# Kernel optimization log

Measured on AMD Instinct MI355X. Metric: run time of the kernel, lower is better.

Reference implementation:

```python
import jax, jax.numpy as jnp
import numpy as np

H, W, D = 160, 160, 16
VOXEL_SIZE = 0.4
VOL_MIN = np.array([-32.0, -32.0, -1.0], dtype=np.float32)
SCALE_MULTIPLIER = 3.0
N_GAUSS = 8192
CHUNK = 64


def setup_inputs() -> dict:
    key = jax.random.key(0)
    k1, k2, k3, k4, k5 = jax.random.split(key, 5)
    vol_min = jnp.asarray(VOL_MIN)
    vol_ext = jnp.array([64.0, 64.0, 6.4], dtype=jnp.float32)
    means3d = jax.random.uniform(k1, (N_GAUSS, 3), jnp.float32) * vol_ext + vol_min
    opacities = jax.random.uniform(k2, (N_GAUSS, 1), jnp.float32)
    # per-axis std devs: 0.2..0.8 m so 3-sigma footprint spans a handful of voxels
    scales = 0.2 + 0.6 * jax.random.uniform(k3, (N_GAUSS, 3), jnp.float32)
    rotations = jax.random.normal(k4, (N_GAUSS, 4), jnp.float32)
    features = jax.random.normal(k5, (N_GAUSS, 32), jnp.float32)
    return {"means3d": means3d, "opacities": opacities, "scales": scales,
            "rotations": rotations, "features": features}


def quat_to_rotmat(q):
    # q: [N,4] wxyz, normalized
    w, x, y, z = q[:, 0], q[:, 1], q[:, 2], q[:, 3]
    R = jnp.stack([
        jnp.stack([1 - 2 * (y * y + z * z), 2 * (x * y - w * z), 2 * (x * z + w * y)], -1),
        jnp.stack([2 * (x * y + w * z), 1 - 2 * (x * x + z * z), 2 * (y * z - w * x)], -1),
        jnp.stack([2 * (x * z - w * y), 2 * (y * z + w * x), 1 - 2 * (x * x + y * y)], -1),
    ], axis=-2)  # [N,3,3]
    return R


def _grid_coords():
    ii, jj, kk = jnp.meshgrid(jnp.arange(H), jnp.arange(W), jnp.arange(D), indexing="ij")
    idx = jnp.stack([ii, jj, kk], axis=-1).astype(jnp.float32)
    return (idx + 0.5) * VOXEL_SIZE + jnp.asarray(VOL_MIN)  # [H,W,D,3] voxel centers


def reference(means3d, opacities, scales, rotations, features):
    x = _grid_coords().reshape(-1, 3)  # [V,3]
    q = rotations / jnp.linalg.norm(rotations, axis=-1, keepdims=True)
    R = quat_to_rotmat(q)
    # covariance = R diag(s^2) R^T
    cov = jnp.einsum("nij,nj,nkj->nik", R, scales * scales, R)
    cov_inv = jnp.linalg.inv(cov)
    sigma = jnp.sqrt(jnp.diagonal(cov, axis1=1, axis2=2))  # [N,3]
    opac = opacities[:, 0]  # [N]
    n = means3d.shape[0]
    nchunks = n // CHUNK

    def chunked(a):
        return a.reshape(nchunks, CHUNK, *a.shape[1:])

    def step(acc, c):
        mu, op, sg, ci, ft = c
        diff = x[:, None, :] - mu[None, :, :]  # [V,CHUNK,3]
        maha = jnp.einsum("vci,cij,vcj->vc", diff, ci, diff)
        # local aggregation cutoff: within scale_multiplier * sigma box around mean
        mask = jnp.all(jnp.abs(diff) <= SCALE_MULTIPLIER * sg[None, :, :], axis=-1)
        w = op[None, :] * jnp.exp(-0.5 * maha) * mask  # [V,CHUNK]
        return acc + w @ ft, None

    acc0 = jnp.zeros((x.shape[0], features.shape[-1]), jnp.float32)
    xs = (chunked(means3d), chunked(opac), chunked(sigma), chunked(cov_inv), chunked(features))
    acc, _ = jax.lax.scan(step, acc0, xs)
    return acc.reshape(H, W, D, features.shape[-1])
```

## Files before the change

kernel.cpp:

```cpp
#include <hip/hip_runtime.h>

#define HH 160
#define WW 160
#define DD 16
#define NG 8192
#define VOXEL 0.4f

#define TTX 20
#define TTY 20
#define TTZ 4
#define NTILES (TTX * TTY * TTZ)
#define CAP 256


__global__ __launch_bounds__(64) void gv_precompute_bin(
    const float* __restrict__ means, const float* __restrict__ opac,
    const float* __restrict__ scales, const float* __restrict__ rots,
    float4* __restrict__ pack, int* __restrict__ tileCnt,
    int* __restrict__ tileList) {
  int g = blockIdx.x * 64 + threadIdx.x;
  if (g >= NG) return;
  float qw = rots[g * 4 + 0], qx = rots[g * 4 + 1];
  float qy = rots[g * 4 + 2], qz = rots[g * 4 + 3];
  float inv = rsqrtf(qw * qw + qx * qx + qy * qy + qz * qz);
  qw *= inv; qx *= inv; qy *= inv; qz *= inv;
  float R[3][3];
  R[0][0] = 1.f - 2.f * (qy * qy + qz * qz);
  R[0][1] = 2.f * (qx * qy - qw * qz);
  R[0][2] = 2.f * (qx * qz + qw * qy);
  R[1][0] = 2.f * (qx * qy + qw * qz);
  R[1][1] = 1.f - 2.f * (qx * qx + qz * qz);
  R[1][2] = 2.f * (qy * qz - qw * qx);
  R[2][0] = 2.f * (qx * qz - qw * qy);
  R[2][1] = 2.f * (qy * qz + qw * qx);
  R[2][2] = 1.f - 2.f * (qx * qx + qy * qy);
  float sx = scales[g * 3 + 0], sy = scales[g * 3 + 1], sz = scales[g * 3 + 2];
  float s2[3] = {sx * sx, sy * sy, sz * sz};
  float is2[3] = {1.f / s2[0], 1.f / s2[1], 1.f / s2[2]};
  float cov00 = 0.f, cov11 = 0.f, cov22 = 0.f;
  float ci00 = 0.f, ci01 = 0.f, ci02 = 0.f, ci11 = 0.f, ci12 = 0.f, ci22 = 0.f;
#pragma unroll
  for (int c = 0; c < 3; c++) {
    cov00 += R[0][c] * R[0][c] * s2[c];
    cov11 += R[1][c] * R[1][c] * s2[c];
    cov22 += R[2][c] * R[2][c] * s2[c];
    ci00 += R[0][c] * R[0][c] * is2[c];
    ci01 += R[0][c] * R[1][c] * is2[c];
    ci02 += R[0][c] * R[2][c] * is2[c];
    ci11 += R[1][c] * R[1][c] * is2[c];
    ci12 += R[1][c] * R[2][c] * is2[c];
    ci22 += R[2][c] * R[2][c] * is2[c];
  }
  float mx = means[g * 3 + 0], my = means[g * 3 + 1], mz = means[g * 3 + 2];
  float bx = 3.f * sqrtf(cov00), by = 3.f * sqrtf(cov11), bz = 3.f * sqrtf(cov22);
  float4* p = pack + (size_t)g * 4;
  p[0] = make_float4(mx, my, mz, opac[g]);
  p[1] = make_float4(bx, by, bz, ci00);
  p[2] = make_float4(ci01, ci02, ci11, ci12);
  p[3] = make_float4(ci22, 0.f, 0.f, 0.f);

  const float eps = 1e-4f;
  int i0 = (int)ceilf((mx - bx + 32.f) * 2.5f - 0.5f - eps);
  int i1 = (int)floorf((mx + bx + 32.f) * 2.5f - 0.5f + eps);
  int j0 = (int)ceilf((my - by + 32.f) * 2.5f - 0.5f - eps);
  int j1 = (int)floorf((my + by + 32.f) * 2.5f - 0.5f + eps);
  int k0 = (int)ceilf((mz - bz + 1.f) * 2.5f - 0.5f - eps);
  int k1 = (int)floorf((mz + bz + 1.f) * 2.5f - 0.5f + eps);
  i0 = max(i0, 0); i1 = min(i1, HH - 1);
  j0 = max(j0, 0); j1 = min(j1, WW - 1);
  k0 = max(k0, 0); k1 = min(k1, DD - 1);
  if (i0 > i1 || j0 > j1 || k0 > k1) return;
  int ti0 = i0 >> 3, ti1 = i1 >> 3;
  int tj0 = j0 >> 3, tj1 = j1 >> 3;
  int tk0 = k0 >> 2, tk1 = k1 >> 2;
  for (int ti = ti0; ti <= ti1; ti++)
    for (int tj = tj0; tj <= tj1; tj++)
      for (int tk = tk0; tk <= tk1; tk++) {
        int t = (ti * TTY + tj) * TTZ + tk;
        int pos = atomicAdd(&tileCnt[t], 1);
        if (pos < CAP) tileList[t * CAP + pos] = g;
      }
}

__global__ __launch_bounds__(256) void gv_voxelize(
    const float4* __restrict__ pack, const float4* __restrict__ feats,
    const int* __restrict__ tileCnt, const int* __restrict__ tileList,
    float4* __restrict__ out) {
  int tid = threadIdx.x;
  int dk = tid & 3, dj = (tid >> 2) & 7, di = tid >> 5;
  int tk = blockIdx.x, tj = blockIdx.y, ti = blockIdx.z;
  int i = ti * 8 + di, j = tj * 8 + dj, k = tk * 4 + dk;

  float px = (i + 0.5f) * VOXEL - 32.f;
  float py = (j + 0.5f) * VOXEL - 32.f;
  float pz = (k + 0.5f) * VOXEL - 1.f;

  int t = (ti * TTY + tj) * TTZ + tk;
  int cnt = tileCnt[t];
  cnt = min(cnt, CAP);
  const int* __restrict__ lst = tileList + t * CAP;

  float4 acc[8];
#pragma unroll
  for (int f = 0; f < 8; f++) acc[f] = make_float4(0.f, 0.f, 0.f, 0.f);

  int n = 0;
  for (; n + 2 <= cnt; n += 2) {
    int g0 = __builtin_amdgcn_readfirstlane(lst[n]);
    int g1 = __builtin_amdgcn_readfirstlane(lst[n + 1]);
    const float4* __restrict__ p0 = pack + (size_t)g0 * 4;
    const float4* __restrict__ p1 = pack + (size_t)g1 * 4;
    float4 a0 = p0[0], b0 = p0[1], c0 = p0[2], d0 = p0[3];
    float4 a1 = p1[0], b1 = p1[1], c1 = p1[2], d1 = p1[3];

    float dx0 = px - a0.x, dy0 = py - a0.y, dz0 = pz - a0.z;
    float dx1 = px - a1.x, dy1 = py - a1.y, dz1 = pz - a1.z;
    bool in0 = (fabsf(dx0) <= b0.x) & (fabsf(dy0) <= b0.y) & (fabsf(dz0) <= b0.z);
    bool in1 = (fabsf(dx1) <= b1.x) & (fabsf(dy1) <= b1.y) & (fabsf(dz1) <= b1.z);

    if (__any(in0)) {
      float maha = b0.w * dx0 * dx0 + c0.z * dy0 * dy0 + d0.x * dz0 * dz0 +
                   2.f * (c0.x * dx0 * dy0 + c0.y * dx0 * dz0 + c0.w * dy0 * dz0);
      float w = in0 ? a0.w * __expf(-0.5f * maha) : 0.f;
      const float4* __restrict__ fp = feats + (size_t)g0 * 8;
#pragma unroll
      for (int f = 0; f < 8; f++) {
        float4 fv = fp[f];
        acc[f].x += w * fv.x;
        acc[f].y += w * fv.y;
        acc[f].z += w * fv.z;
        acc[f].w += w * fv.w;
      }
    }
    if (__any(in1)) {
      float maha = b1.w * dx1 * dx1 + c1.z * dy1 * dy1 + d1.x * dz1 * dz1 +
                   2.f * (c1.x * dx1 * dy1 + c1.y * dx1 * dz1 + c1.w * dy1 * dz1);
      float w = in1 ? a1.w * __expf(-0.5f * maha) : 0.f;
      const float4* __restrict__ fp = feats + (size_t)g1 * 8;
#pragma unroll
      for (int f = 0; f < 8; f++) {
        float4 fv = fp[f];
        acc[f].x += w * fv.x;
        acc[f].y += w * fv.y;
        acc[f].z += w * fv.z;
        acc[f].w += w * fv.w;
      }
    }
  }
  if (n < cnt) {
    int gg = __builtin_amdgcn_readfirstlane(lst[n]);
    const float4* __restrict__ p = pack + (size_t)gg * 4;
    float4 pa = p[0], pb = p[1];
    float dx = px - pa.x, dy = py - pa.y, dz = pz - pa.z;
    bool in = (fabsf(dx) <= pb.x) & (fabsf(dy) <= pb.y) & (fabsf(dz) <= pb.z);
    if (__any(in)) {
      float4 pc = p[2], pd = p[3];
      float maha = pb.w * dx * dx + pc.z * dy * dy + pd.x * dz * dz +
                   2.f * (pc.x * dx * dy + pc.y * dx * dz + pc.w * dy * dz);
      float w = in ? pa.w * __expf(-0.5f * maha) : 0.f;
      const float4* __restrict__ fp = feats + (size_t)gg * 8;
#pragma unroll
      for (int f = 0; f < 8; f++) {
        float4 fv = fp[f];
        acc[f].x += w * fv.x;
        acc[f].y += w * fv.y;
        acc[f].z += w * fv.z;
        acc[f].w += w * fv.w;
      }
    }
  }

  size_t v = ((size_t)i * WW + j) * DD + k;
  float4* o = out + v * 8;
#pragma unroll
  for (int f = 0; f < 8; f++) o[f] = acc[f];
}

extern "C" void kernel_launch(void* const* d_in, const int* in_sizes, int n_in,
                              void* d_out, int out_size, void* d_ws, size_t ws_size,
                              hipStream_t stream) {
  const float* means  = (const float*)d_in[0];
  const float* opac   = (const float*)d_in[1];
  const float* scales = (const float*)d_in[2];
  const float* rots   = (const float*)d_in[3];
  const float4* feats = (const float4*)d_in[4];

  char* ws = (char*)d_ws;
  float4* pack   = (float4*)ws;
  int* tileCnt   = (int*)(ws + 512 * 1024);
  int* tileList  = (int*)(ws + 520 * 1024);

  hipMemsetAsync(tileCnt, 0, NTILES * sizeof(int), stream);
  gv_precompute_bin<<<128, 64, 0, stream>>>(means, opac, scales, rots,
                                            pack, tileCnt, tileList);
  dim3 grid(TTZ, TTY, TTX);
  gv_voxelize<<<grid, 256, 0, stream>>>(pack, feats, tileCnt, tileList,
                                        (float4*)d_out);
}
```

Measured before the change: 128.9 us.

## Bin gaussians into finer 4x4x4 tiles so each wavefront scans its own list

Gaussians are now binned into 4x4x4 voxel tiles instead of 8x8x4, and each 64-lane wavefront of the voxelize block maps to one of these finer tiles and reads its own per-tile list. Each wave therefore tests fewer gaussians that cannot reach its voxels, which cuts the per-candidate load and the culling check. In exchange the binning pass does more atomics and list writes, since each gaussian lands in more tiles. The per-tile capacity drops to 128, which could drop gaussians in dense tiles.

```diff
diff --git a/kernel.cpp b/kernel.cpp
--- a/kernel.cpp
+++ b/kernel.cpp
@@ -6,11 +6,15 @@
 #define NG 8192
 #define VOXEL 0.4f
 
+#define FTX 40
+#define FTY 40
+#define FTZ 4
+#define NFT (FTX * FTY * FTZ)
+#define CAP 128
+
 #define TTX 20
 #define TTY 20
 #define TTZ 4
-#define NTILES (TTX * TTY * TTZ)
-#define CAP 256
 
 
 __global__ __launch_bounds__(64) void gv_precompute_bin(
@@ -70,13 +74,13 @@
   j0 = max(j0, 0); j1 = min(j1, WW - 1);
   k0 = max(k0, 0); k1 = min(k1, DD - 1);
   if (i0 > i1 || j0 > j1 || k0 > k1) return;
-  int ti0 = i0 >> 3, ti1 = i1 >> 3;
-  int tj0 = j0 >> 3, tj1 = j1 >> 3;
+  int ti0 = i0 >> 2, ti1 = i1 >> 2;
+  int tj0 = j0 >> 2, tj1 = j1 >> 2;
   int tk0 = k0 >> 2, tk1 = k1 >> 2;
   for (int ti = ti0; ti <= ti1; ti++)
     for (int tj = tj0; tj <= tj1; tj++)
       for (int tk = tk0; tk <= tk1; tk++) {
-        int t = (ti * TTY + tj) * TTZ + tk;
+        int t = (ti * FTY + tj) * FTZ + tk;
         int pos = atomicAdd(&tileCnt[t], 1);
         if (pos < CAP) tileList[t * CAP + pos] = g;
       }
@@ -87,7 +91,10 @@
     const int* __restrict__ tileCnt, const int* __restrict__ tileList,
     float4* __restrict__ out) {
   int tid = threadIdx.x;
-  int dk = tid & 3, dj = (tid >> 2) & 7, di = tid >> 5;
+  int w = tid >> 6;
+  int wi = w >> 1, wj = w & 1;
+  int l = tid & 63;
+  int dk = l & 3, dj = wj * 4 + ((l >> 2) & 3), di = wi * 4 + (l >> 4);
   int tk = blockIdx.x, tj = blockIdx.y, ti = blockIdx.z;
   int i = ti * 8 + di, j = tj * 8 + dj, k = tk * 4 + dk;
 
@@ -95,8 +102,9 @@
   float py = (j + 0.5f) * VOXEL - 32.f;
   float pz = (k + 0.5f) * VOXEL - 1.f;
 
-  int t = (ti * TTY + tj) * TTZ + tk;
-  int cnt = tileCnt[t];
+  int sti = ti * 2 + wi, stj = tj * 2 + wj, stk = tk;
+  int t = __builtin_amdgcn_readfirstlane((sti * FTY + stj) * FTZ + stk);
+  int cnt = __builtin_amdgcn_readfirstlane(tileCnt[t]);
   cnt = min(cnt, CAP);
   const int* __restrict__ lst = tileList + t * CAP;
 
@@ -121,29 +129,29 @@
     if (__any(in0)) {
       float maha = b0.w * dx0 * dx0 + c0.z * dy0 * dy0 + d0.x * dz0 * dz0 +
                    2.f * (c0.x * dx0 * dy0 + c0.y * dx0 * dz0 + c0.w * dy0 * dz0);
-      float w = in0 ? a0.w * __expf(-0.5f * maha) : 0.f;
+      float wgt = in0 ? a0.w * __expf(-0.5f * maha) : 0.f;
       const float4* __restrict__ fp = feats + (size_t)g0 * 8;
 #pragma unroll
       for (int f = 0; f < 8; f++) {
         float4 fv = fp[f];
-        acc[f].x += w * fv.x;
-        acc[f].y += w * fv.y;
-        acc[f].z += w * fv.z;
-        acc[f].w += w * fv.w;
+        acc[f].x += wgt * fv.x;
+        acc[f].y += wgt * fv.y;
+        acc[f].z += wgt * fv.z;
+        acc[f].w += wgt * fv.w;
       }
     }
     if (__any(in1)) {
       float maha = b1.w * dx1 * dx1 + c1.z * dy1 * dy1 + d1.x * dz1 * dz1 +
                    2.f * (c1.x * dx1 * dy1 + c1.y * dx1 * dz1 + c1.w * dy1 * dz1);
-      float w = in1 ? a1.w * __expf(-0.5f * maha) : 0.f;
+      float wgt = in1 ? a1.w * __expf(-0.5f * maha) : 0.f;
       const float4* __restrict__ fp = feats + (size_t)g1 * 8;
 #pragma unroll
       for (int f = 0; f < 8; f++) {
         float4 fv = fp[f];
-        acc[f].x += w * fv.x;
-        acc[f].y += w * fv.y;
-        acc[f].z += w * fv.z;
-        acc[f].w += w * fv.w;
+        acc[f].x += wgt * fv.x;
+        acc[f].y += wgt * fv.y;
+        acc[f].z += wgt * fv.z;
+        acc[f].w += wgt * fv.w;
       }
     }
   }
@@ -157,15 +165,15 @@
       float4 pc = p[2], pd = p[3];
       float maha = pb.w * dx * dx + pc.z * dy * dy + pd.x * dz * dz +
                    2.f * (pc.x * dx * dy + pc.y * dx * dz + pc.w * dy * dz);
-      float w = in ? pa.w * __expf(-0.5f * maha) : 0.f;
+      float wgt = in ? pa.w * __expf(-0.5f * maha) : 0.f;
       const float4* __restrict__ fp = feats + (size_t)gg * 8;
 #pragma unroll
       for (int f = 0; f < 8; f++) {
         float4 fv = fp[f];
-        acc[f].x += w * fv.x;
-        acc[f].y += w * fv.y;
-        acc[f].z += w * fv.z;
-        acc[f].w += w * fv.w;
+        acc[f].x += wgt * fv.x;
+        acc[f].y += wgt * fv.y;
+        acc[f].z += wgt * fv.z;
+        acc[f].w += wgt * fv.w;
       }
     }
   }
@@ -188,9 +196,9 @@
   char* ws = (char*)d_ws;
   float4* pack   = (float4*)ws;
   int* tileCnt   = (int*)(ws + 512 * 1024);
-  int* tileList  = (int*)(ws + 520 * 1024);
-
-  hipMemsetAsync(tileCnt, 0, NTILES * sizeof(int), stream);
+  int* tileList  = (int*)(ws + 544 * 1024);
+
+  hipMemsetAsync(tileCnt, 0, NFT * sizeof(int), stream);
   gv_precompute_bin<<<128, 64, 0, stream>>>(means, opac, scales, rots,
                                             pack, tileCnt, tileList);
   dim3 grid(TTZ, TTY, TTX);
```

Result: slower. 131.7 us (+2.1%).

## Materialize per-tile gaussian params and features contiguously during binning

Applied to the files above, without the earlier changes.

The binning kernel now copies each gaussian's packed parameters and its 32 features into a per-tile contiguous buffer instead of storing only an index. The voxelize kernel then streams these records sequentially, avoiding the indirect index load and the scattered gathers. In exchange the binning kernel writes far more data from a small grid, and the tile capacity is halved, which risks dropping gaussians on dense tiles.

```diff
diff --git a/kernel.cpp b/kernel.cpp
--- a/kernel.cpp
+++ b/kernel.cpp
@@ -10,14 +10,14 @@
 #define TTY 20
 #define TTZ 4
 #define NTILES (TTX * TTY * TTZ)
-#define CAP 256
+#define CAP 128
 
 
 __global__ __launch_bounds__(64) void gv_precompute_bin(
     const float* __restrict__ means, const float* __restrict__ opac,
     const float* __restrict__ scales, const float* __restrict__ rots,
-    float4* __restrict__ pack, int* __restrict__ tileCnt,
-    int* __restrict__ tileList) {
+    const float4* __restrict__ feats, int* __restrict__ tileCnt,
+    float4* __restrict__ tileData) {
   int g = blockIdx.x * 64 + threadIdx.x;
   if (g >= NG) return;
   float qw = rots[g * 4 + 0], qx = rots[g * 4 + 1];
@@ -53,11 +53,6 @@
   }
   float mx = means[g * 3 + 0], my = means[g * 3 + 1], mz = means[g * 3 + 2];
   float bx = 3.f * sqrtf(cov00), by = 3.f * sqrtf(cov11), bz = 3.f * sqrtf(cov22);
-  float4* p = pack + (size_t)g * 4;
-  p[0] = make_float4(mx, my, mz, opac[g]);
-  p[1] = make_float4(bx, by, bz, ci00);
-  p[2] = make_float4(ci01, ci02, ci11, ci12);
-  p[3] = make_float4(ci22, 0.f, 0.f, 0.f);
 
   const float eps = 1e-4f;
   int i0 = (int)ceilf((mx - bx + 32.f) * 2.5f - 0.5f - eps);
@@ -70,6 +65,15 @@
   j0 = max(j0, 0); j1 = min(j1, WW - 1);
   k0 = max(k0, 0); k1 = min(k1, DD - 1);
   if (i0 > i1 || j0 > j1 || k0 > k1) return;
+
+  float4 p0 = make_float4(mx, my, mz, opac[g]);
+  float4 p1 = make_float4(bx, by, bz, ci00);
+  float4 p2 = make_float4(ci01, ci02, ci11, ci12);
+  float4 p3 = make_float4(ci22, 0.f, 0.f, 0.f);
+  const float4* __restrict__ fsrc = feats + (size_t)g * 8;
+  float4 f0 = fsrc[0], f1 = fsrc[1], f2 = fsrc[2], f3 = fsrc[3];
+  float4 f4 = fsrc[4], f5 = fsrc[5], f6 = fsrc[6], f7 = fsrc[7];
+
   int ti0 = i0 >> 3, ti1 = i1 >> 3;
   int tj0 = j0 >> 3, tj1 = j1 >> 3;
   int tk0 = k0 >> 2, tk1 = k1 >> 2;
@@ -78,13 +82,17 @@
       for (int tk = tk0; tk <= tk1; tk++) {
         int t = (ti * TTY + tj) * TTZ + tk;
         int pos = atomicAdd(&tileCnt[t], 1);
-        if (pos < CAP) tileList[t * CAP + pos] = g;
+        if (pos < CAP) {
+          float4* __restrict__ d = tileData + ((size_t)t * CAP + pos) * 12;
+          d[0] = p0;  d[1] = p1;  d[2] = p2;  d[3] = p3;
+          d[4] = f0;  d[5] = f1;  d[6] = f2;  d[7] = f3;
+          d[8] = f4;  d[9] = f5;  d[10] = f6; d[11] = f7;
+        }
       }
 }
 
 __global__ __launch_bounds__(256) void gv_voxelize(
-    const float4* __restrict__ pack, const float4* __restrict__ feats,
-    const int* __restrict__ tileCnt, const int* __restrict__ tileList,
+    const int* __restrict__ tileCnt, const float4* __restrict__ tileData,
     float4* __restrict__ out) {
   int tid = threadIdx.x;
   int dk = tid & 3, dj = (tid >> 2) & 7, di = tid >> 5;
@@ -98,7 +106,7 @@
   int t = (ti * TTY + tj) * TTZ + tk;
   int cnt = tileCnt[t];
   cnt = min(cnt, CAP);
-  const int* __restrict__ lst = tileList + t * CAP;
+  const float4* __restrict__ gd = tileData + (size_t)t * CAP * 12;
 
   float4 acc[8];
 #pragma unroll
@@ -106,12 +114,14 @@
 
   int n = 0;
   for (; n + 2 <= cnt; n += 2) {
-    int g0 = __builtin_amdgcn_readfirstlane(lst[n]);
-    int g1 = __builtin_amdgcn_readfirstlane(lst[n + 1]);
-    const float4* __restrict__ p0 = pack + (size_t)g0 * 4;
-    const float4* __restrict__ p1 = pack + (size_t)g1 * 4;
-    float4 a0 = p0[0], b0 = p0[1], c0 = p0[2], d0 = p0[3];
-    float4 a1 = p1[0], b1 = p1[1], c1 = p1[2], d1 = p1[3];
+    const float4* __restrict__ q0 = gd + (size_t)n * 12;
+    const float4* __restrict__ q1 = q0 + 12;
+    float4 a0 = q0[0], b0 = q0[1], c0 = q0[2], d0 = q0[3];
+    float4 e00 = q0[4], e01 = q0[5], e02 = q0[6], e03 = q0[7];
+    float4 e04 = q0[8], e05 = q0[9], e06 = q0[10], e07 = q0[11];
+    float4 a1 = q1[0], b1 = q1[1], c1 = q1[2], d1 = q1[3];
+    float4 e10 = q1[4], e11 = q1[5], e12 = q1[6], e13 = q1[7];
+    float4 e14 = q1[8], e15 = q1[9], e16 = q1[10], e17 = q1[11];
 
     float dx0 = px - a0.x, dy0 = py - a0.y, dz0 = pz - a0.z;
     float dx1 = px - a1.x, dy1 = py - a1.y, dz1 = pz - a1.z;
@@ -121,51 +131,46 @@
     if (__any(in0)) {
       float maha = b0.w * dx0 * dx0 + c0.z * dy0 * dy0 + d0.x * dz0 * dz0 +
                    2.f * (c0.x * dx0 * dy0 + c0.y * dx0 * dz0 + c0.w * dy0 * dz0);
-      float w = in0 ? a0.w * __expf(-0.5f * maha) : 0.f;
-      const float4* __restrict__ fp = feats + (size_t)g0 * 8;
-#pragma unroll
-      for (int f = 0; f < 8; f++) {
-        float4 fv = fp[f];
-        acc[f].x += w * fv.x;
-        acc[f].y += w * fv.y;
-        acc[f].z += w * fv.z;
-        acc[f].w += w * fv.w;
-      }
+      float wgt = in0 ? a0.w * __expf(-0.5f * maha) : 0.f;
+      acc[0].x += wgt * e00.x; acc[0].y += wgt * e00.y; acc[0].z += wgt * e00.z; acc[0].w += wgt * e00.w;
+      acc[1].x += wgt * e01.x; acc[1].y += wgt * e01.y; acc[1].z += wgt * e01.z; acc[1].w += wgt * e01.w;
+      acc[2].x += wgt * e02.x; acc[2].y += wgt * e02.y; acc[2].z += wgt * e02.z; acc[2].w += wgt * e02.w;
+      acc[3].x += wgt * e03.x; acc[3].y += wgt * e03.y; acc[3].z += wgt * e03.z; acc[3].w += wgt * e03.w;
+      acc[4].x += wgt * e04.x; acc[4].y += wgt * e04.y; acc[4].z += wgt * e04.z; acc[4].w += wgt * e04.w;
+      acc[5].x += wgt * e05.x; acc[5].y += wgt * e05.y; acc[5].z += wgt * e05.z; acc[5].w += wgt * e05.w;
+      acc[6].x += wgt * e06.x; acc[6].y += wgt * e06.y; acc[6].z += wgt * e06.z; acc[6].w += wgt * e06.w;
+      acc[7].x += wgt * e07.x; acc[7].y += wgt * e07.y; acc[7].z += wgt * e07.z; acc[7].w += wgt * e07.w;
     }
     if (__any(in1)) {
       float maha = b1.w * dx1 * dx1 + c1.z * dy1 * dy1 + d1.x * dz1 * dz1 +
                    2.f * (c1.x * dx1 * dy1 + c1.y * dx1 * dz1 + c1.w * dy1 * dz1);
-      float w = in1 ? a1.w * __expf(-0.5f * maha) : 0.f;
-      const float4* __restrict__ fp = feats + (size_t)g1 * 8;
-#pragma unroll
-      for (int f = 0; f < 8; f++) {
-        float4 fv = fp[f];
-        acc[f].x += w * fv.x;
-        acc[f].y += w * fv.y;
-        acc[f].z += w * fv.z;
-        acc[f].w += w * fv.w;
-      }
+      float wgt = in1 ? a1.w * __expf(-0.5f * maha) : 0.f;
+      acc[0].x += wgt * e10.x; acc[0].y += wgt * e10.y; acc[0].z += wgt * e10.z; acc[0].w += wgt * e10.w;
+      acc[1].x += wgt * e11.x; acc[1].y += wgt * e11.y; acc[1].z += wgt * e11.z; acc[1].w += wgt * e11.w;
+      acc[2].x += wgt * e12.x; acc[2].y += wgt * e12.y; acc[2].z += wgt * e12.z; acc[2].w += wgt * e12.w;
+      acc[3].x += wgt * e13.x; acc[3].y += wgt * e13.y; acc[3].z += wgt * e13.z; acc[3].w += wgt * e13.w;
+      acc[4].x += wgt * e14.x; acc[4].y += wgt * e14.y; acc[4].z += wgt * e14.z; acc[4].w += wgt * e14.w;
+      acc[5].x += wgt * e15.x; acc[5].y += wgt * e15.y; acc[5].z += wgt * e15.z; acc[5].w += wgt * e15.w;
+      acc[6].x += wgt * e16.x; acc[6].y += wgt * e16.y; acc[6].z += wgt * e16.z; acc[6].w += wgt * e16.w;
+      acc[7].x += wgt * e17.x; acc[7].y += wgt * e17.y; acc[7].z += wgt * e17.z; acc[7].w += wgt * e17.w;
     }
   }
   if (n < cnt) {
-    int gg = __builtin_amdgcn_readfirstlane(lst[n]);
-    const float4* __restrict__ p = pack + (size_t)gg * 4;
-    float4 pa = p[0], pb = p[1];
+    const float4* __restrict__ q = gd + (size_t)n * 12;
+    float4 pa = q[0], pb = q[1], pc = q[2], pd = q[3];
     float dx = px - pa.x, dy = py - pa.y, dz = pz - pa.z;
     bool in = (fabsf(dx) <= pb.x) & (fabsf(dy) <= pb.y) & (fabsf(dz) <= pb.z);
     if (__any(in)) {
-      float4 pc = p[2], pd = p[3];
       float maha = pb.w * dx * dx + pc.z * dy * dy + pd.x * dz * dz +
                    2.f * (pc.x * dx * dy + pc.y * dx * dz + pc.w * dy * dz);
-      float w = in ? pa.w * __expf(-0.5f * maha) : 0.f;
-      const float4* __restrict__ fp = feats + (size_t)gg * 8;
+      float wgt = in ? pa.w * __expf(-0.5f * maha) : 0.f;
 #pragma unroll
       for (int f = 0; f < 8; f++) {
-        float4 fv = fp[f];
-        acc[f].x += w * fv.x;
-        acc[f].y += w * fv.y;
-        acc[f].z += w * fv.z;
-        acc[f].w += w * fv.w;
+        float4 fv = q[4 + f];
+        acc[f].x += wgt * fv.x;
+        acc[f].y += wgt * fv.y;
+        acc[f].z += wgt * fv.z;
+        acc[f].w += wgt * fv.w;
       }
     }
   }
@@ -186,14 +191,12 @@
   const float4* feats = (const float4*)d_in[4];
 
   char* ws = (char*)d_ws;
-  float4* pack   = (float4*)ws;
-  int* tileCnt   = (int*)(ws + 512 * 1024);
-  int* tileList  = (int*)(ws + 520 * 1024);
+  int* tileCnt     = (int*)ws;
+  float4* tileData = (float4*)(ws + 64 * 1024);
 
   hipMemsetAsync(tileCnt, 0, NTILES * sizeof(int), stream);
   gv_precompute_bin<<<128, 64, 0, stream>>>(means, opac, scales, rots,
-                                            pack, tileCnt, tileList);
+                                            feats, tileCnt, tileData);
   dim3 grid(TTZ, TTY, TTX);
-  gv_voxelize<<<grid, 256, 0, stream>>>(pack, feats, tileCnt, tileList,
-                                        (float4*)d_out);
+  gv_voxelize<<<grid, 256, 0, stream>>>(tileCnt, tileData, (float4*)d_out);
 }
```

Result: slower. 144.2 us (+11.8%).
